# Optimization experiments

Hardware: AMD Instinct MI355X
Metric: run time of the kernel (lower is better)

The kernel has to match this reference:

```python
import jax, jax.numpy as jnp
import numpy as np

N0, N1, N2, N3 = 200000, 50000, 12000, 3000
E0, E1, E2 = 500000, 120000, 30000
D_IN, D_H, D_OUT = 256, 256, 64


def setup_inputs() -> dict:
    key = jax.random.key(0)
    ks = jax.random.split(key, 16)
    s = 1.0 / np.sqrt(D_IN)
    return {
        "x": jax.random.normal(ks[0], (N0, D_IN), jnp.float32),
        "src0": jax.random.randint(ks[1], (E0,), 0, N0),
        "dst0": jax.random.randint(ks[2], (E0,), 0, N1),
        "src1": jax.random.randint(ks[3], (E1,), 0, N1),
        "dst1": jax.random.randint(ks[4], (E1,), 0, N2),
        "src2": jax.random.randint(ks[5], (E2,), 0, N2),
        "dst2": jax.random.randint(ks[6], (E2,), 0, N3),
        "num_dst0": N1, "num_dst1": N2, "num_dst2": N3,
        "Ws0": jax.random.normal(ks[7], (D_IN, D_H), jnp.float32) * s,
        "Wn0": jax.random.normal(ks[8], (D_IN, D_H), jnp.float32) * s,
        "b0": jnp.zeros((D_H,), jnp.float32),
        "Ws1": jax.random.normal(ks[9], (D_H, D_H), jnp.float32) * s,
        "Wn1": jax.random.normal(ks[10], (D_H, D_H), jnp.float32) * s,
        "b1": jnp.zeros((D_H,), jnp.float32),
        "Ws2": jax.random.normal(ks[11], (D_H, D_OUT), jnp.float32) * s,
        "Wn2": jax.random.normal(ks[12], (D_H, D_OUT), jnp.float32) * s,
        "b2": jnp.zeros((D_OUT,), jnp.float32),
    }


def sage_conv(src, dst, num_dst, h_src, Wn, Ws, b):
    # DGL SAGEConv(mean): fc_self(h_dst) + fc_neigh(mean_{in-edges} h_src) + bias
    h_dst = h_src[:num_dst]
    msg = h_src[src]                                          # [E, d] gather
    agg = jax.ops.segment_sum(msg, dst, num_segments=num_dst)  # [num_dst, d]
    deg = jax.ops.segment_sum(jnp.ones((dst.shape[0],), h_src.dtype), dst,
                              num_segments=num_dst)
    h_neigh = agg / jnp.maximum(deg, 1.0)[:, None]
    return h_dst @ Ws + h_neigh @ Wn + b


def reference(x, src0, dst0, src1, dst1, src2, dst2,
              num_dst0, num_dst1, num_dst2,
              Ws0, Wn0, b0, Ws1, Wn1, b1, Ws2, Wn2, b2):
    h = sage_conv(src0, dst0, num_dst0, x, Wn0, Ws0, b0)       # layer 0 (no act, per source)
    h = sage_conv(src1, dst1, num_dst1, h, Wn1, Ws1, b1)       # layer 1
    h = jax.nn.relu(h)                                         # activation after middle layer
    # dropout omitted (eval / deterministic mode)
    h = sage_conv(src2, dst2, num_dst2, h, Wn2, Ws2, b2)       # layer 2
    return h
```

## Files before the change

### kernel.cpp

```cpp
#include <hip/hip_runtime.h>

#define N0_SRC 200000
#define N1_DST 50000
#define N2_DST 12000
#define N3_DST 3000
#define DH 256
#define DOUT 64

typedef __attribute__((ext_vector_type(8))) short short8;
typedef __attribute__((ext_vector_type(4))) float f32x4;

__device__ __forceinline__ ushort f2bf(float f) {
    union { float f; uint32_t u; } v; v.f = f;
    uint32_t r = (v.u + 0x7FFF + ((v.u >> 16) & 1)) >> 16;
    return (ushort)r;
}
__device__ __forceinline__ float bf2f(ushort u) {
    union { uint32_t u; float f; } v; v.u = ((uint32_t)u) << 16;
    return v.f;
}

__global__ void f32_to_bf16_kernel(const float* __restrict__ in,
                                   ushort* __restrict__ out, long n) {
    long i = ((long)blockIdx.x * 256 + threadIdx.x) * 4;
    if (i >= n) return;
    float4 v = *(const float4*)(in + i);
    ushort4 o;
    o.x = f2bf(v.x); o.y = f2bf(v.y); o.z = f2bf(v.z); o.w = f2bf(v.w);
    *(ushort4*)(out + i) = o;
}

__global__ void transpose_w_all(const float* __restrict__ W0, const float* __restrict__ W1,
                                const float* __restrict__ W2, const float* __restrict__ W3,
                                const float* __restrict__ W4, const float* __restrict__ W5,
                                ushort* __restrict__ out) {
    const float* W; int Ndim; ushort* o;
    switch (blockIdx.y) {
        case 0: W = W0; Ndim = 256; o = out; break;
        case 1: W = W1; Ndim = 256; o = out + 65536; break;
        case 2: W = W2; Ndim = 256; o = out + 131072; break;
        case 3: W = W3; Ndim = 256; o = out + 196608; break;
        case 4: W = W4; Ndim = 64;  o = out + 262144; break;
        default: W = W5; Ndim = 64; o = out + 278528; break;
    }
    int id = blockIdx.x * 256 + threadIdx.x;
    int n = id >> 8;
    int k = id & 255;
    if (n >= Ndim) return;
    o[id] = f2bf(W[k * Ndim + n]);
}

__global__ void hist_kernel(const int* __restrict__ dst, int* __restrict__ cnt, int E) {
    int e = blockIdx.x * 256 + threadIdx.x;
    if (e < E) atomicAdd(&cnt[dst[e]], 1);
}

__global__ void scan_phase_a(const int* __restrict__ cnt, int* __restrict__ partial, int n) {
    __shared__ int red[4];
    int t = threadIdx.x;
    int i = blockIdx.x * 1024 + t * 4;
    int s = 0;
    if (i + 3 < n) {
        int4 v = *(const int4*)(cnt + i);
        s = v.x + v.y + v.z + v.w;
    }
#pragma unroll
    for (int d = 32; d; d >>= 1) s += __shfl_down(s, d, 64);
    if ((t & 63) == 0) red[t >> 6] = s;
    __syncthreads();
    if (t == 0) partial[blockIdx.x] = red[0] + red[1] + red[2] + red[3];
}

__global__ void scan_phase_b(int* __restrict__ partial, int nb) {
    int t = threadIdx.x;
    int own = (t < nb) ? partial[t] : 0;
    int v = own;
#pragma unroll
    for (int d = 1; d < 64; d <<= 1) {
        int u = __shfl_up(v, d, 64);
        if (t >= d) v += u;
    }
    if (t < nb) partial[t] = v - own;
}

__global__ void scan_phase_c(const int* __restrict__ cnt, const int* __restrict__ partial,
                             int* __restrict__ off, int* __restrict__ cursor, int n) {
    __shared__ int tsum[256];
    int t = threadIdx.x;
    int i = blockIdx.x * 1024 + t * 4;
    int4 c = make_int4(0, 0, 0, 0);
    if (i + 3 < n) c = *(const int4*)(cnt + i);
    int s = c.x + c.y + c.z + c.w;
    tsum[t] = s;
    __syncthreads();
#pragma unroll
    for (int d = 1; d < 256; d <<= 1) {
        int u = (t >= d) ? tsum[t - d] : 0;
        __syncthreads();
        tsum[t] += u;
        __syncthreads();
    }
    int base = partial[blockIdx.x] + tsum[t] - s;
    if (i + 3 < n) {
        int4 ov;
        ov.x = base;
        ov.y = ov.x + c.x;
        ov.z = ov.y + c.y;
        ov.w = ov.z + c.z;
        *(int4*)(off + i) = ov;
        *(int4*)(cursor + i) = ov;
        if (i + 4 == n) off[n] = ov.w + c.w;
    }
}

__global__ void fill_kernel(const int* __restrict__ src, const int* __restrict__ dst,
                            int* __restrict__ cursor, int* __restrict__ eidx, int E) {
    int e = blockIdx.x * 256 + threadIdx.x;
    if (e < E) {
        int p = atomicAdd(&cursor[dst[e]], 1);
        eidx[p] = src[e];
    }
}

__global__ void gather_mean_bf16_kernel(const ushort* __restrict__ h,
                                        const int* __restrict__ off,
                                        const int* __restrict__ eidx,
                                        ushort* __restrict__ hn,
                                        int num_dst) {
    int w = blockIdx.x * 4 + (threadIdx.x >> 6);
    int lane = threadIdx.x & 63;
    if (w >= num_dst) return;
    int beg = off[w];
    int end = off[w + 1];
    float a0 = 0.f, a1 = 0.f, a2 = 0.f, a3 = 0.f;
    int i = beg;
    for (; i + 1 < end; i += 2) {
        int s0 = eidx[i];
        int s1 = eidx[i + 1];
        ushort4 v0 = ((const ushort4*)(h + (size_t)s0 * DH))[lane];
        ushort4 v1 = ((const ushort4*)(h + (size_t)s1 * DH))[lane];
        a0 += bf2f(v0.x) + bf2f(v1.x);
        a1 += bf2f(v0.y) + bf2f(v1.y);
        a2 += bf2f(v0.z) + bf2f(v1.z);
        a3 += bf2f(v0.w) + bf2f(v1.w);
    }
    if (i < end) {
        int s0 = eidx[i];
        ushort4 v0 = ((const ushort4*)(h + (size_t)s0 * DH))[lane];
        a0 += bf2f(v0.x); a1 += bf2f(v0.y); a2 += bf2f(v0.z); a3 += bf2f(v0.w);
    }
    float inv = 1.0f / fmaxf((float)(end - beg), 1.0f);
    ushort4 o;
    o.x = f2bf(a0 * inv); o.y = f2bf(a1 * inv);
    o.z = f2bf(a2 * inv); o.w = f2bf(a3 * inv);
    *(ushort4*)(hn + (size_t)w * DH + lane * 4) = o;
}

template <bool RELU, bool OUT_BF16>
__global__ void gemm_mfma(const ushort* __restrict__ Ad,
                          const ushort* __restrict__ An,
                          const ushort* __restrict__ Wst,
                          const ushort* __restrict__ Wnt,
                          const float* __restrict__ bias,
                          void* __restrict__ Cv,
                          int M, int N) {
    const int K = 256;
    const int LDK = 40;
    __shared__ ushort As[128 * LDK];
    __shared__ ushort Bs[64 * LDK];

    int tid  = threadIdx.x;
    int lane = tid & 63;
    int wid  = tid >> 6;
    int quad = lane >> 4;
    int mr   = lane & 15;
    int row0 = blockIdx.y * 128;
    int col0 = blockIdx.x * 64;

    f32x4 acc[2][4];
#pragma unroll
    for (int i = 0; i < 2; ++i)
#pragma unroll
        for (int j = 0; j < 4; ++j) acc[i][j] = (f32x4){0.f, 0.f, 0.f, 0.f};

    for (int pass = 0; pass < 2; ++pass) {
        const ushort* A  = pass ? An : Ad;
        const ushort* Wt = pass ? Wnt : Wst;
        for (int k0 = 0; k0 < K; k0 += 32) {
#pragma unroll
            for (int c = 0; c < 2; ++c) {
                int chunk = tid + c * 256;
                int r   = chunk >> 2;
                int seg = chunk & 3;
                int row = row0 + r;
                uint4 v = make_uint4(0u, 0u, 0u, 0u);
                if (row < M) v = *(const uint4*)(A + (size_t)row * K + k0 + seg * 8);
                *(uint4*)(&As[r * LDK + seg * 8]) = v;
            }
            {
                int n   = tid >> 2;
                int seg = tid & 3;
                uint4 v = *(const uint4*)(Wt + (size_t)(col0 + n) * K + k0 + seg * 8);
                *(uint4*)(&Bs[n * LDK + seg * 8]) = v;
            }
            __syncthreads();
            short8 a[2], b[4];
#pragma unroll
            for (int mt = 0; mt < 2; ++mt)
                a[mt] = *(const short8*)(&As[(wid * 32 + mt * 16 + mr) * LDK + quad * 8]);
#pragma unroll
            for (int nt = 0; nt < 4; ++nt)
                b[nt] = *(const short8*)(&Bs[(nt * 16 + mr) * LDK + quad * 8]);
#pragma unroll
            for (int mt = 0; mt < 2; ++mt)
#pragma unroll
                for (int nt = 0; nt < 4; ++nt)
                    acc[mt][nt] = __builtin_amdgcn_mfma_f32_16x16x32_bf16(
                        a[mt], b[nt], acc[mt][nt], 0, 0, 0);
            __syncthreads();
        }
    }

#pragma unroll
    for (int mt = 0; mt < 2; ++mt) {
#pragma unroll
        for (int i = 0; i < 4; ++i) {
            int row = row0 + wid * 32 + mt * 16 + quad * 4 + i;
            if (row >= M) continue;
#pragma unroll
            for (int nt = 0; nt < 4; ++nt) {
                int col = col0 + nt * 16 + mr;
                float v = acc[mt][nt][i] + bias[col];
                if (RELU) v = fmaxf(v, 0.0f);
                if (OUT_BF16) ((ushort*)Cv)[(size_t)row * N + col] = f2bf(v);
                else          ((float*)Cv)[(size_t)row * N + col] = v;
            }
        }
    }
}

static void build_csr(const int* src, const int* dst, int E, int num_dst,
                      int* cnt, int* off, int* cursor, int* eidx, int* partial,
                      hipStream_t stream) {
    int nb = (num_dst + 1023) / 1024;
    hipMemsetAsync(cnt, 0, num_dst * sizeof(int), stream);
    hist_kernel<<<(E + 255) / 256, 256, 0, stream>>>(dst, cnt, E);
    scan_phase_a<<<nb, 256, 0, stream>>>(cnt, partial, num_dst);
    scan_phase_b<<<1, 64, 0, stream>>>(partial, nb);
    scan_phase_c<<<nb, 256, 0, stream>>>(cnt, partial, off, cursor, num_dst);
    fill_kernel<<<(E + 255) / 256, 256, 0, stream>>>(src, dst, cursor, eidx, E);
}

extern "C" void kernel_launch(void* const* d_in, const int* in_sizes, int n_in,
                              void* d_out, int out_size, void* d_ws, size_t ws_size,
                              hipStream_t stream) {
    const float* x    = (const float*)d_in[0];
    const int* src0   = (const int*)d_in[1];
    const int* dst0   = (const int*)d_in[2];
    const int* src1   = (const int*)d_in[3];
    const int* dst1   = (const int*)d_in[4];
    const int* src2   = (const int*)d_in[5];
    const int* dst2   = (const int*)d_in[6];
    const float* Ws0  = (const float*)d_in[10];
    const float* Wn0  = (const float*)d_in[11];
    const float* b0   = (const float*)d_in[12];
    const float* Ws1  = (const float*)d_in[13];
    const float* Wn1  = (const float*)d_in[14];
    const float* b1   = (const float*)d_in[15];
    const float* Ws2  = (const float*)d_in[16];
    const float* Wn2  = (const float*)d_in[17];
    const float* b2   = (const float*)d_in[18];
    float* out = (float*)d_out;

    int E0 = in_sizes[1];
    int E1 = in_sizes[3];
    int E2 = in_sizes[5];

    ushort* wsu  = (ushort*)d_ws;
    ushort* xb   = wsu;
    ushort* hn0b = xb   + (size_t)N0_SRC * DH;
    ushort* h1b  = hn0b + (size_t)N1_DST * DH;
    ushort* hn1b = h1b  + (size_t)N1_DST * DH;
    ushort* h2b  = hn1b + (size_t)N2_DST * DH;
    ushort* hn2b = h2b  + (size_t)N2_DST * DH;
    ushort* Wt   = hn2b + (size_t)N3_DST * DH;
    ushort* Ws0t = Wt;
    ushort* Wn0t = Wt + 65536;
    ushort* Ws1t = Wt + 131072;
    ushort* Wn1t = Wt + 196608;
    ushort* Ws2t = Wt + 262144;
    ushort* Wn2t = Wt + 278528;
    int* cnt     = (int*)(Wt + 294912);
    int* off     = cnt + N1_DST;
    int* cursor  = off + N1_DST + 4;
    int* eidx    = cursor + N1_DST;
    int* partial = eidx + 500000;

    long nxb = (long)N0_SRC * DH;
    f32_to_bf16_kernel<<<(int)((nxb / 4 + 255) / 256), 256, 0, stream>>>(x, xb, nxb);
    transpose_w_all<<<dim3(256, 6), 256, 0, stream>>>(Ws0, Wn0, Ws1, Wn1, Ws2, Wn2, Wt);

    build_csr(src0, dst0, E0, N1_DST, cnt, off, cursor, eidx, partial, stream);
    gather_mean_bf16_kernel<<<(N1_DST + 3) / 4, 256, 0, stream>>>(xb, off, eidx, hn0b, N1_DST);
    {
        dim3 g(DH / 64, (N1_DST + 127) / 128);
        gemm_mfma<false, true><<<g, 256, 0, stream>>>(xb, hn0b, Ws0t, Wn0t, b0, h1b, N1_DST, DH);
    }

    build_csr(src1, dst1, E1, N2_DST, cnt, off, cursor, eidx, partial, stream);
    gather_mean_bf16_kernel<<<(N2_DST + 3) / 4, 256, 0, stream>>>(h1b, off, eidx, hn1b, N2_DST);
    {
        dim3 g(DH / 64, (N2_DST + 127) / 128);
        gemm_mfma<true, true><<<g, 256, 0, stream>>>(h1b, hn1b, Ws1t, Wn1t, b1, h2b, N2_DST, DH);
    }

    build_csr(src2, dst2, E2, N3_DST, cnt, off, cursor, eidx, partial, stream);
    gather_mean_bf16_kernel<<<(N3_DST + 3) / 4, 256, 0, stream>>>(h2b, off, eidx, hn2b, N3_DST);
    {
        dim3 g(DOUT / 64, (N3_DST + 127) / 128);
        gemm_mfma<false, false><<<g, 256, 0, stream>>>(h2b, hn2b, Ws2t, Wn2t, b2, out, N3_DST, DOUT);
    }
}
```

Before: 570.6 us.

## Build all three layers' CSR in one batched pass, widen GEMM tile and gather unroll

Merges the three per-layer CSR builds into one set of launches by offsetting destination ids into a combined count/offset array, so the memset, histogram, scan and fill kernels run once instead of three times. The gather-mean loop is unrolled to four neighbors per iteration for more memory-level parallelism. The GEMM gains a BN template parameter and uses 128-wide column tiles for the 256-wide layers, halving the number of times A tiles are reloaded. The larger tile uses more registers and LDS and yields fewer blocks, and the batched CSR needs a bigger workspace.

```diff
diff --git a/kernel.cpp b/kernel.cpp
--- a/kernel.cpp
+++ b/kernel.cpp
@@ -4,8 +4,10 @@
 #define N1_DST 50000
 #define N2_DST 12000
 #define N3_DST 3000
+#define NTOT_DST 65000
 #define DH 256
 #define DOUT 64
+#define EMAX_TOT 650000
 
 typedef __attribute__((ext_vector_type(8))) short short8;
 typedef __attribute__((ext_vector_type(4))) float f32x4;
@@ -50,9 +52,33 @@
     o[id] = f2bf(W[k * Ndim + n]);
 }
 
-__global__ void hist_kernel(const int* __restrict__ dst, int* __restrict__ cnt, int E) {
+__global__ void hist3_kernel(const int* __restrict__ d0, int E0,
+                             const int* __restrict__ d1, int E1,
+                             const int* __restrict__ d2, int E2,
+                             int* __restrict__ cnt) {
+    int layer = blockIdx.y;
+    const int* dst; int E; int base;
+    if (layer == 0)      { dst = d0; E = E0; base = 0; }
+    else if (layer == 1) { dst = d1; E = E1; base = N1_DST; }
+    else                 { dst = d2; E = E2; base = N1_DST + N2_DST; }
     int e = blockIdx.x * 256 + threadIdx.x;
-    if (e < E) atomicAdd(&cnt[dst[e]], 1);
+    if (e < E) atomicAdd(&cnt[base + dst[e]], 1);
+}
+
+__global__ void fill3_kernel(const int* __restrict__ s0, const int* __restrict__ d0, int E0,
+                             const int* __restrict__ s1, const int* __restrict__ d1, int E1,
+                             const int* __restrict__ s2, const int* __restrict__ d2, int E2,
+                             int* __restrict__ cursor, int* __restrict__ eidx) {
+    int layer = blockIdx.y;
+    const int* src; const int* dst; int E; int base;
+    if (layer == 0)      { src = s0; dst = d0; E = E0; base = 0; }
+    else if (layer == 1) { src = s1; dst = d1; E = E1; base = N1_DST; }
+    else                 { src = s2; dst = d2; E = E2; base = N1_DST + N2_DST; }
+    int e = blockIdx.x * 256 + threadIdx.x;
+    if (e < E) {
+        int p = atomicAdd(&cursor[base + dst[e]], 1);
+        eidx[p] = src[e];
+    }
 }
 
 __global__ void scan_phase_a(const int* __restrict__ cnt, int* __restrict__ partial, int n) {
@@ -110,15 +136,6 @@
         *(int4*)(off + i) = ov;
         *(int4*)(cursor + i) = ov;
         if (i + 4 == n) off[n] = ov.w + c.w;
-    }
-}
-
-__global__ void fill_kernel(const int* __restrict__ src, const int* __restrict__ dst,
-                            int* __restrict__ cursor, int* __restrict__ eidx, int E) {
-    int e = blockIdx.x * 256 + threadIdx.x;
-    if (e < E) {
-        int p = atomicAdd(&cursor[dst[e]], 1);
-        eidx[p] = src[e];
     }
 }
 
@@ -134,17 +151,18 @@
     int end = off[w + 1];
     float a0 = 0.f, a1 = 0.f, a2 = 0.f, a3 = 0.f;
     int i = beg;
-    for (; i + 1 < end; i += 2) {
-        int s0 = eidx[i];
-        int s1 = eidx[i + 1];
+    for (; i + 3 < end; i += 4) {
+        int s0 = eidx[i], s1 = eidx[i + 1], s2 = eidx[i + 2], s3 = eidx[i + 3];
         ushort4 v0 = ((const ushort4*)(h + (size_t)s0 * DH))[lane];
         ushort4 v1 = ((const ushort4*)(h + (size_t)s1 * DH))[lane];
-        a0 += bf2f(v0.x) + bf2f(v1.x);
-        a1 += bf2f(v0.y) + bf2f(v1.y);
-        a2 += bf2f(v0.z) + bf2f(v1.z);
-        a3 += bf2f(v0.w) + bf2f(v1.w);
-    }
-    if (i < end) {
+        ushort4 v2 = ((const ushort4*)(h + (size_t)s2 * DH))[lane];
+        ushort4 v3 = ((const ushort4*)(h + (size_t)s3 * DH))[lane];
+        a0 += (bf2f(v0.x) + bf2f(v1.x)) + (bf2f(v2.x) + bf2f(v3.x));
+        a1 += (bf2f(v0.y) + bf2f(v1.y)) + (bf2f(v2.y) + bf2f(v3.y));
+        a2 += (bf2f(v0.z) + bf2f(v1.z)) + (bf2f(v2.z) + bf2f(v3.z));
+        a3 += (bf2f(v0.w) + bf2f(v1.w)) + (bf2f(v2.w) + bf2f(v3.w));
+    }
+    for (; i < end; ++i) {
         int s0 = eidx[i];
         ushort4 v0 = ((const ushort4*)(h + (size_t)s0 * DH))[lane];
         a0 += bf2f(v0.x); a1 += bf2f(v0.y); a2 += bf2f(v0.z); a3 += bf2f(v0.w);
@@ -156,7 +174,7 @@
     *(ushort4*)(hn + (size_t)w * DH + lane * 4) = o;
 }
 
-template <bool RELU, bool OUT_BF16>
+template <int BN, bool RELU, bool OUT_BF16>
 __global__ void gemm_mfma(const ushort* __restrict__ Ad,
                           const ushort* __restrict__ An,
                           const ushort* __restrict__ Wst,
@@ -166,8 +184,9 @@
                           int M, int N) {
     const int K = 256;
     const int LDK = 40;
+    const int NT = BN / 16;
     __shared__ ushort As[128 * LDK];
-    __shared__ ushort Bs[64 * LDK];
+    __shared__ ushort Bs[BN * LDK];
 
     int tid  = threadIdx.x;
     int lane = tid & 63;
@@ -175,13 +194,13 @@
     int quad = lane >> 4;
     int mr   = lane & 15;
     int row0 = blockIdx.y * 128;
-    int col0 = blockIdx.x * 64;
-
-    f32x4 acc[2][4];
+    int col0 = blockIdx.x * BN;
+
+    f32x4 acc[2][NT];
 #pragma unroll
     for (int i = 0; i < 2; ++i)
 #pragma unroll
-        for (int j = 0; j < 4; ++j) acc[i][j] = (f32x4){0.f, 0.f, 0.f, 0.f};
+        for (int j = 0; j < NT; ++j) acc[i][j] = (f32x4){0.f, 0.f, 0.f, 0.f};
 
     for (int pass = 0; pass < 2; ++pass) {
         const ushort* A  = pass ? An : Ad;
@@ -197,24 +216,26 @@
                 if (row < M) v = *(const uint4*)(A + (size_t)row * K + k0 + seg * 8);
                 *(uint4*)(&As[r * LDK + seg * 8]) = v;
             }
-            {
-                int n   = tid >> 2;
-                int seg = tid & 3;
+#pragma unroll
+            for (int c = 0; c < BN / 64; ++c) {
+                int chunk = tid + c * 256;
+                int n   = chunk >> 2;
+                int seg = chunk & 3;
                 uint4 v = *(const uint4*)(Wt + (size_t)(col0 + n) * K + k0 + seg * 8);
                 *(uint4*)(&Bs[n * LDK + seg * 8]) = v;
             }
             __syncthreads();
-            short8 a[2], b[4];
+            short8 a[2], b[NT];
 #pragma unroll
             for (int mt = 0; mt < 2; ++mt)
                 a[mt] = *(const short8*)(&As[(wid * 32 + mt * 16 + mr) * LDK + quad * 8]);
 #pragma unroll
-            for (int nt = 0; nt < 4; ++nt)
+            for (int nt = 0; nt < NT; ++nt)
                 b[nt] = *(const short8*)(&Bs[(nt * 16 + mr) * LDK + quad * 8]);
 #pragma unroll
             for (int mt = 0; mt < 2; ++mt)
 #pragma unroll
-                for (int nt = 0; nt < 4; ++nt)
+                for (int nt = 0; nt < NT; ++nt)
                     acc[mt][nt] = __builtin_amdgcn_mfma_f32_16x16x32_bf16(
                         a[mt], b[nt], acc[mt][nt], 0, 0, 0);
             __syncthreads();
@@ -228,7 +249,7 @@
             int row = row0 + wid * 32 + mt * 16 + quad * 4 + i;
             if (row >= M) continue;
 #pragma unroll
-            for (int nt = 0; nt < 4; ++nt) {
+            for (int nt = 0; nt < NT; ++nt) {
                 int col = col0 + nt * 16 + mr;
                 float v = acc[mt][nt][i] + bias[col];
                 if (RELU) v = fmaxf(v, 0.0f);
@@ -237,18 +258,6 @@
             }
         }
     }
-}
-
-static void build_csr(const int* src, const int* dst, int E, int num_dst,
-                      int* cnt, int* off, int* cursor, int* eidx, int* partial,
-                      hipStream_t stream) {
-    int nb = (num_dst + 1023) / 1024;
-    hipMemsetAsync(cnt, 0, num_dst * sizeof(int), stream);
-    hist_kernel<<<(E + 255) / 256, 256, 0, stream>>>(dst, cnt, E);
-    scan_phase_a<<<nb, 256, 0, stream>>>(cnt, partial, num_dst);
-    scan_phase_b<<<1, 64, 0, stream>>>(partial, nb);
-    scan_phase_c<<<nb, 256, 0, stream>>>(cnt, partial, off, cursor, num_dst);
-    fill_kernel<<<(E + 255) / 256, 256, 0, stream>>>(src, dst, cursor, eidx, E);
 }
 
 extern "C" void kernel_launch(void* const* d_in, const int* in_sizes, int n_in,
@@ -291,33 +300,44 @@
     ushort* Ws2t = Wt + 262144;
     ushort* Wn2t = Wt + 278528;
     int* cnt     = (int*)(Wt + 294912);
-    int* off     = cnt + N1_DST;
-    int* cursor  = off + N1_DST + 4;
-    int* eidx    = cursor + N1_DST;
-    int* partial = eidx + 500000;
+    int* off     = cnt + NTOT_DST;
+    int* cursor  = off + NTOT_DST + 4;
+    int* eidx    = cursor + NTOT_DST;
+    int* partial = eidx + EMAX_TOT;
 
     long nxb = (long)N0_SRC * DH;
     f32_to_bf16_kernel<<<(int)((nxb / 4 + 255) / 256), 256, 0, stream>>>(x, xb, nxb);
     transpose_w_all<<<dim3(256, 6), 256, 0, stream>>>(Ws0, Wn0, Ws1, Wn1, Ws2, Wn2, Wt);
 
-    build_csr(src0, dst0, E0, N1_DST, cnt, off, cursor, eidx, partial, stream);
-    gather_mean_bf16_kernel<<<(N1_DST + 3) / 4, 256, 0, stream>>>(xb, off, eidx, hn0b, N1_DST);
+    int Emax = max(max(E0, E1), E2);
+    int nb = (NTOT_DST + 1023) / 1024;
+    hipMemsetAsync(cnt, 0, NTOT_DST * sizeof(int), stream);
+    hist3_kernel<<<dim3((Emax + 255) / 256, 3), 256, 0, stream>>>(dst0, E0, dst1, E1, dst2, E2, cnt);
+    scan_phase_a<<<nb, 256, 0, stream>>>(cnt, partial, NTOT_DST);
+    scan_phase_b<<<1, 64, 0, stream>>>(partial, nb);
+    scan_phase_c<<<nb, 256, 0, stream>>>(cnt, partial, off, cursor, NTOT_DST);
+    fill3_kernel<<<dim3((Emax + 255) / 256, 3), 256, 0, stream>>>(
+        src0, dst0, E0, src1, dst1, E1, src2, dst2, E2, cursor, eidx);
+
+    const int* off0 = off;
+    const int* off1 = off + N1_DST;
+    const int* off2 = off + N1_DST + N2_DST;
+
+    gather_mean_bf16_kernel<<<(N1_DST + 3) / 4, 256, 0, stream>>>(xb, off0, eidx, hn0b, N1_DST);
     {
-        dim3 g(DH / 64, (N1_DST + 127) / 128);
-        gemm_mfma<false, true><<<g, 256, 0, stream>>>(xb, hn0b, Ws0t, Wn0t, b0, h1b, N1_DST, DH);
-    }
-
-    build_csr(src1, dst1, E1, N2_DST, cnt, off, cursor, eidx, partial, stream);
-    gather_mean_bf16_kernel<<<(N2_DST + 3) / 4, 256, 0, stream>>>(h1b, off, eidx, hn1b, N2_DST);
+        dim3 g(DH / 128, (N1_DST + 127) / 128);
+        gemm_mfma<128, false, true><<<g, 256, 0, stream>>>(xb, hn0b, Ws0t, Wn0t, b0, h1b, N1_DST, DH);
+    }
+
+    gather_mean_bf16_kernel<<<(N2_DST + 3) / 4, 256, 0, stream>>>(h1b, off1, eidx, hn1b, N2_DST);
     {
-        dim3 g(DH / 64, (N2_DST + 127) / 128);
-        gemm_mfma<true, true><<<g, 256, 0, stream>>>(h1b, hn1b, Ws1t, Wn1t, b1, h2b, N2_DST, DH);
-    }
-
-    build_csr(src2, dst2, E2, N3_DST, cnt, off, cursor, eidx, partial, stream);
-    gather_mean_bf16_kernel<<<(N3_DST + 3) / 4, 256, 0, stream>>>(h2b, off, eidx, hn2b, N3_DST);
+        dim3 g(DH / 128, (N2_DST + 127) / 128);
+        gemm_mfma<128, true, true><<<g, 256, 0, stream>>>(h1b, hn1b, Ws1t, Wn1t, b1, h2b, N2_DST, DH);
+    }
+
+    gather_mean_bf16_kernel<<<(N3_DST + 3) / 4, 256, 0, stream>>>(h2b, off2, eidx, hn2b, N3_DST);
     {
         dim3 g(DOUT / 64, (N3_DST + 127) / 128);
-        gemm_mfma<false, false><<<g, 256, 0, stream>>>(h2b, hn2b, Ws2t, Wn2t, b2, out, N3_DST, DOUT);
-    }
-}
+        gemm_mfma<64, false, false><<<g, 256, 0, stream>>>(h2b, hn2b, Ws2t, Wn2t, b2, out, N3_DST, DOUT);
+    }
+}
```

New measurement: 523.5 us. -8.3%, faster.
